# Kernel tuning notes

Hardware: AMD Instinct MI355X
Metric: run time of the kernel (lower is better)

## Reference

```python
import jax, jax.numpy as jnp
import numpy as np

N_NODES = 100000


def setup_inputs() -> dict:
    key = jax.random.key(0)
    ks = jax.random.split(key, 8)
    E = 1600000
    x = jax.random.normal(ks[0], (N_NODES, 128), dtype=jnp.float32)
    src = jax.random.randint(ks[1], (E,), 0, N_NODES, dtype=jnp.int32)
    dst = jax.random.randint(ks[2], (E,), 0, N_NODES, dtype=jnp.int32)
    s = 1.0 / np.sqrt(128.0)
    w_self = jax.random.normal(ks[3], (5, 128, 128), dtype=jnp.float32) * s
    w_neigh = jax.random.normal(ks[4], (5, 128, 128), dtype=jnp.float32) * s
    b = jnp.zeros((5, 128), dtype=jnp.float32)
    w_self_out = jax.random.normal(ks[5], (128, 47), dtype=jnp.float32) * s
    w_neigh_out = jax.random.normal(ks[6], (128, 47), dtype=jnp.float32) * s
    b_out = jnp.zeros((47,), dtype=jnp.float32)
    return {"x": x, "src": src, "dst": dst, "w_self": w_self, "w_neigh": w_neigh,
            "b": b, "w_self_out": w_self_out, "w_neigh_out": w_neigh_out, "b_out": b_out}


def _mean_agg(h, src, dst, inv_deg):
    # segment-sum of source features into destination nodes, then mean
    summed = jax.ops.segment_sum(h[src], dst, num_segments=N_NODES)  # [N, d]
    return summed * inv_deg[:, None]


def _sage_layer(h, src, dst, inv_deg, ws, wn, bias):
    neigh = _mean_agg(h, src, dst, inv_deg)
    return h @ ws + neigh @ wn + bias


def reference(x, src, dst, w_self, w_neigh, b, w_self_out, w_neigh_out, b_out):
    # in-degree, clamped to 1 for isolated nodes (DGL mean aggregator behavior)
    deg = jax.ops.segment_sum(jnp.ones_like(dst, dtype=x.dtype), dst, num_segments=N_NODES)
    inv_deg = 1.0 / jnp.maximum(deg, 1.0)

    # layer 0: no ReLU after (matches original forward)
    h = _sage_layer(x, src, dst, inv_deg, w_self[0], w_neigh[0], b[0])
    # layers 1..4: SAGEConv + ReLU
    for i in range(1, 5):
        h = _sage_layer(h, src, dst, inv_deg, w_self[i], w_neigh[i], b[i])
        h = jax.nn.relu(h)
    # final layer: 128 -> num_classes, no activation
    h = _sage_layer(h, src, dst, inv_deg, w_self_out, w_neigh_out, b_out)
    return h
```

## Files before the change

### kernel.cpp

```cpp
#include <hip/hip_runtime.h>

typedef float f4 __attribute__((ext_vector_type(4)));
typedef float f32x4 __attribute__((ext_vector_type(4)));
typedef short s16x8 __attribute__((ext_vector_type(8)));

#define N_NODES 100000
#define NBUCK 196
#define NB1 256

__device__ inline unsigned short f2bf(float f) {
    unsigned int u = __builtin_bit_cast(unsigned int, f);
    u += 0x7FFFu + ((u >> 16) & 1u);
    return (unsigned short)(u >> 16);
}
__device__ inline float bflo(unsigned int v) { return __builtin_bit_cast(float, v << 16); }
__device__ inline float bfhi(unsigned int v) { return __builtin_bit_cast(float, v & 0xFFFF0000u); }


__global__ __launch_bounds__(256) void k_hist(const int* __restrict__ dst,
                                              int* __restrict__ histG, int E) {
    __shared__ int h[NBUCK];
    int tid = threadIdx.x;
    for (int i = tid; i < NBUCK; i += 256) h[i] = 0;
    __syncthreads();
    int chunk = (E + NB1 - 1) / NB1;
    int s = blockIdx.x * chunk, eN = min(E, s + chunk);
    for (int i = s + tid; i < eN; i += 256) atomicAdd(&h[dst[i] >> 9], 1);
    __syncthreads();
    for (int i = tid; i < NBUCK; i += 256) histG[i * NB1 + blockIdx.x] = h[i];
}

__global__ __launch_bounds__(1024) void k_scanB(int* __restrict__ histG) {
    __shared__ int ps[1024];
    int t = threadIdx.x;
    int base = t * 49;
    int vals[49];
    int sum = 0;
#pragma unroll
    for (int i = 0; i < 49; ++i) { vals[i] = histG[base + i]; sum += vals[i]; }
    ps[t] = sum;
    __syncthreads();
    for (int off = 1; off < 1024; off <<= 1) {
        int v = (t >= off) ? ps[t - off] : 0;
        __syncthreads();
        ps[t] += v;
        __syncthreads();
    }
    int run = ps[t] - sum;
#pragma unroll
    for (int i = 0; i < 49; ++i) { int v = vals[i]; histG[base + i] = run; run += v; }
}

__global__ __launch_bounds__(256) void k_place(const int* __restrict__ src,
                                               const int* __restrict__ dst,
                                               const int* __restrict__ histG,
                                               unsigned int* __restrict__ ebuf, int E) {
    __shared__ int cur[NBUCK];
    int tid = threadIdx.x;
    for (int i = tid; i < NBUCK; i += 256) cur[i] = histG[i * NB1 + blockIdx.x];
    __syncthreads();
    int chunk = (E + NB1 - 1) / NB1;
    int s = blockIdx.x * chunk, eN = min(E, s + chunk);
    for (int i = s + tid; i < eN; i += 256) {
        int d = dst[i];
        int b = d >> 9;
        int pos = atomicAdd(&cur[b], 1);
        ebuf[pos] = (unsigned int)src[i] | ((unsigned int)(d & 511) << 17);
    }
}

__global__ __launch_bounds__(256) void k_csr(const unsigned int* __restrict__ ebuf,
                                             const int* __restrict__ histG,
                                             int* __restrict__ rp, int* __restrict__ col,
                                             float* __restrict__ invd, int N, int E) {
    __shared__ int ldeg[512];
    __shared__ int lbase[512];
    int b = blockIdx.x, tid = threadIdx.x;
    int base = histG[b * NB1];
    int endB = (b == NBUCK - 1) ? E : histG[(b + 1) * NB1];
    int cnt = endB - base;
    int n0 = b << 9;

    ldeg[tid] = 0;
    ldeg[tid + 256] = 0;
    __syncthreads();
    for (int i = tid; i < cnt; i += 256) atomicAdd(&ldeg[ebuf[base + i] >> 17], 1);
    __syncthreads();

    int a0 = ldeg[tid], a1 = ldeg[tid + 256];
    lbase[tid] = a0;
    lbase[tid + 256] = a1;
    __syncthreads();
    for (int off = 1; off < 512; off <<= 1) {
        int v0 = (tid >= off) ? lbase[tid - off] : 0;
        int v1 = (tid + 256 >= off) ? lbase[tid + 256 - off] : 0;
        __syncthreads();
        lbase[tid] += v0;
        lbase[tid + 256] += v1;
        __syncthreads();
    }
    int e0 = lbase[tid] - a0, e1 = lbase[tid + 256] - a1;
    __syncthreads();
    lbase[tid] = e0;
    lbase[tid + 256] = e1;
    ldeg[tid] = 0;
    ldeg[tid + 256] = 0;
    __syncthreads();

    for (int i = tid; i < cnt; i += 256) {
        unsigned int p = ebuf[base + i];
        int dl = p >> 17;
        int pos = base + lbase[dl] + atomicAdd(&ldeg[dl], 1);
        col[pos] = (int)(p & 0x1FFFFu);
    }

    int g0 = n0 + tid, g1 = n0 + tid + 256;
    if (g0 < N) { rp[g0] = base + e0; invd[g0] = 1.0f / fmaxf((float)a0, 1.0f); }
    if (g1 < N) { rp[g1] = base + e1; invd[g1] = 1.0f / fmaxf((float)a1, 1.0f); }
    if (b == NBUCK - 1 && tid == 0) rp[N] = E;
}


__global__ void k_cvt(const float* __restrict__ x, unsigned short* __restrict__ xb, int n8) {
    int t = blockIdx.x * 256 + threadIdx.x;
    if (t >= n8) return;
    f4 a = *(const f4*)&x[(size_t)t * 8];
    f4 b = *(const f4*)&x[(size_t)t * 8 + 4];
    s16x8 p;
    p[0] = (short)f2bf(a[0]); p[1] = (short)f2bf(a[1]);
    p[2] = (short)f2bf(a[2]); p[3] = (short)f2bf(a[3]);
    p[4] = (short)f2bf(b[0]); p[5] = (short)f2bf(b[1]);
    p[6] = (short)f2bf(b[2]); p[7] = (short)f2bf(b[3]);
    *(s16x8*)&xb[(size_t)t * 8] = p;
}

__global__ void k_prepw(const float* __restrict__ ws, const float* __restrict__ wn,
                        unsigned short* __restrict__ wp) {
    int t = blockIdx.x * 256 + threadIdx.x;
    if (t >= 5 * 4096) return;
    int l = t & 63, nfg = (t >> 6) & 7, ks = (t >> 9) & 7, lyr = t >> 12;
    int n = nfg * 16 + (l & 15);
    s16x8 p;
#pragma unroll
    for (int j = 0; j < 8; ++j) {
        int k = ks * 32 + (l >> 4) * 8 + j;
        float v = (k < 128) ? ws[((size_t)lyr * 128 + k) * 128 + n]
                            : wn[((size_t)lyr * 128 + (k - 128)) * 128 + n];
        p[j] = (short)f2bf(v);
    }
    *(s16x8*)&wp[(size_t)t * 8] = p;
}

__global__ void k_prepwo(const float* __restrict__ wso, const float* __restrict__ wno,
                         unsigned short* __restrict__ wpo) {
    int t = blockIdx.x * 256 + threadIdx.x;
    if (t >= 1536) return;
    int l = t & 63, q = t >> 6;
    int nf = q % 3, ks = q / 3;
    int n = nf * 16 + (l & 15);
    s16x8 p;
#pragma unroll
    for (int j = 0; j < 8; ++j) {
        int k = ks * 32 + (l >> 4) * 8 + j;
        float v = 0.f;
        if (n < 47) v = (k < 128) ? wso[(size_t)k * 47 + n] : wno[(size_t)(k - 128) * 47 + n];
        p[j] = (short)f2bf(v);
    }
    *(s16x8*)&wpo[(size_t)t * 8] = p;
}


__global__ __launch_bounds__(256) void k_agg(const unsigned short* __restrict__ h,
                                             const int* __restrict__ rp,
                                             const int* __restrict__ col,
                                             const float* __restrict__ invd,
                                             unsigned short* __restrict__ out, int n) {
    int gw = (blockIdx.x * 256 + threadIdx.x) >> 6;
    int lane = threadIdx.x & 63;
    if (gw >= n) return;
    const unsigned int* hp = (const unsigned int*)h;
    int beg = rp[gw], end = rp[gw + 1];
    float ax = 0.f, ay = 0.f;
    int e = beg;
    for (; e + 8 <= end; e += 8) {
        unsigned int u[8];
#pragma unroll
        for (int i = 0; i < 8; ++i) u[i] = hp[(size_t)col[e + i] * 64 + lane];
#pragma unroll
        for (int i = 0; i < 8; ++i) { ax += bflo(u[i]); ay += bfhi(u[i]); }
    }
    if (e < end) {
        int rem = end - e;
        unsigned int u[8];
#pragma unroll
        for (int i = 0; i < 8; ++i) {
            int idx = (i < rem) ? (e + i) : e;
            u[i] = hp[(size_t)col[idx] * 64 + lane];
        }
#pragma unroll
        for (int i = 0; i < 8; ++i) {
            if (i < rem) { ax += bflo(u[i]); ay += bfhi(u[i]); }
        }
    }
    float iv = invd[gw];
    unsigned int r = (unsigned int)f2bf(ax * iv) | ((unsigned int)f2bf(ay * iv) << 16);
    ((unsigned int*)out)[(size_t)gw * 64 + lane] = r;
}


__global__ __launch_bounds__(256) void gemm128(const unsigned short* __restrict__ h,
                                               const unsigned short* __restrict__ nb,
                                               const unsigned short* __restrict__ wl,
                                               const float* __restrict__ bias,
                                               unsigned short* __restrict__ out,
                                               int M, int relu) {
    __shared__ s16x8 afr[4096];
    const int tid = threadIdx.x;
    const int l = tid & 63, w = tid >> 6;
    const int r0 = blockIdx.x * 128;
    const int cg = (w * 4 + (l >> 4)) * 8;

    s16x8 th[8], tn[8];
#pragma unroll
    for (int i = 0; i < 8; ++i) {
        int r = r0 + i * 16 + (l & 15);
        if (r >= M) r = M - 1;
        th[i] = *(const s16x8*)(h + (size_t)r * 128 + cg);
        tn[i] = *(const s16x8*)(nb + (size_t)r * 128 + cg);
    }
#pragma unroll
    for (int i = 0; i < 8; ++i) {
        afr[(w * 8 + i) * 64 + l] = th[i];
        afr[((w + 4) * 8 + i) * 64 + l] = tn[i];
    }
    __syncthreads();

    const int mh = w >> 1, nh = w & 1;
    const s16x8* wf = (const s16x8*)wl;

    f32x4 acc[4][4];
#pragma unroll
    for (int i = 0; i < 4; ++i)
#pragma unroll
        for (int j = 0; j < 4; ++j) acc[i][j] = (f32x4)0.f;

#pragma unroll
    for (int ks = 0; ks < 8; ++ks) {
        s16x8 bw[4], ha[4];
#pragma unroll
        for (int nf = 0; nf < 4; ++nf) bw[nf] = wf[(ks * 8 + nh * 4 + nf) * 64 + l];
#pragma unroll
        for (int mf = 0; mf < 4; ++mf) ha[mf] = afr[(ks * 8 + mh * 4 + mf) * 64 + l];
#pragma unroll
        for (int mf = 0; mf < 4; ++mf)
#pragma unroll
            for (int nf = 0; nf < 4; ++nf)
                acc[mf][nf] = __builtin_amdgcn_mfma_f32_16x16x32_bf16(bw[nf], ha[mf],
                                                                      acc[mf][nf], 0, 0, 0);
    }

    f4 bv[4];
#pragma unroll
    for (int nf = 0; nf < 4; ++nf)
        bv[nf] = *(const f4*)&bias[nh * 64 + nf * 16 + ((l >> 4) << 2)];

#pragma unroll
    for (int mf = 0; mf < 4; ++mf) {
        int row = r0 + mh * 64 + mf * 16 + (l & 15);
        if (row >= M) continue;
#pragma unroll
        for (int nf = 0; nf < 4; ++nf) {
            int ncol = nh * 64 + nf * 16 + ((l >> 4) << 2);
            f32x4 a = acc[mf][nf];
            float v0 = a[0] + bv[nf][0], v1 = a[1] + bv[nf][1];
            float v2 = a[2] + bv[nf][2], v3 = a[3] + bv[nf][3];
            if (relu) {
                v0 = fmaxf(v0, 0.f); v1 = fmaxf(v1, 0.f);
                v2 = fmaxf(v2, 0.f); v3 = fmaxf(v3, 0.f);
            }
            uint2 p;
            p.x = (unsigned int)f2bf(v0) | ((unsigned int)f2bf(v1) << 16);
            p.y = (unsigned int)f2bf(v2) | ((unsigned int)f2bf(v3) << 16);
            *(uint2*)(out + (size_t)row * 128 + ncol) = p;
        }
    }
}


__global__ __launch_bounds__(256) void gemm_out47(const unsigned short* __restrict__ h,
                                                  const unsigned short* __restrict__ nb,
                                                  const unsigned short* __restrict__ wpo,
                                                  const float* __restrict__ bo,
                                                  float* __restrict__ out, int M) {
    __shared__ s16x8 afr[4096];
    const int tid = threadIdx.x;
    const int l = tid & 63, w = tid >> 6;
    const int r0 = blockIdx.x * 128;
    const int cg = (w * 4 + (l >> 4)) * 8;

    s16x8 th[8], tn[8];
#pragma unroll
    for (int i = 0; i < 8; ++i) {
        int r = r0 + i * 16 + (l & 15);
        if (r >= M) r = M - 1;
        th[i] = *(const s16x8*)(h + (size_t)r * 128 + cg);
        tn[i] = *(const s16x8*)(nb + (size_t)r * 128 + cg);
    }
#pragma unroll
    for (int i = 0; i < 8; ++i) {
        afr[(w * 8 + i) * 64 + l] = th[i];
        afr[((w + 4) * 8 + i) * 64 + l] = tn[i];
    }
    __syncthreads();

    const s16x8* wf = (const s16x8*)wpo;
    f32x4 acc[2][3];
#pragma unroll
    for (int i = 0; i < 2; ++i)
#pragma unroll
        for (int j = 0; j < 3; ++j) acc[i][j] = (f32x4)0.f;

#pragma unroll
    for (int ks = 0; ks < 8; ++ks) {
        s16x8 bw[3], ha[2];
#pragma unroll
        for (int nf = 0; nf < 3; ++nf) bw[nf] = wf[(ks * 3 + nf) * 64 + l];
#pragma unroll
        for (int mf = 0; mf < 2; ++mf) ha[mf] = afr[(ks * 8 + w * 2 + mf) * 64 + l];
#pragma unroll
        for (int mf = 0; mf < 2; ++mf)
#pragma unroll
            for (int nf = 0; nf < 3; ++nf)
                acc[mf][nf] = __builtin_amdgcn_mfma_f32_16x16x32_bf16(bw[nf], ha[mf],
                                                                      acc[mf][nf], 0, 0, 0);
    }

#pragma unroll
    for (int mf = 0; mf < 2; ++mf) {
        int row = r0 + w * 32 + mf * 16 + (l & 15);
        if (row >= M) continue;
#pragma unroll
        for (int nf = 0; nf < 3; ++nf) {
            int ncol = nf * 16 + ((l >> 4) << 2);
            f32x4 a = acc[mf][nf];
#pragma unroll
            for (int jj = 0; jj < 4; ++jj) {
                int n = ncol + jj;
                if (n < 47) out[(size_t)row * 47 + n] = a[jj] + bo[n];
            }
        }
    }
}


static inline char* alignp(char* p) {
    return (char*)(((size_t)p + 255) & ~(size_t)255);
}

extern "C" void kernel_launch(void* const* d_in, const int* in_sizes, int n_in,
                              void* d_out, int out_size, void* d_ws, size_t ws_size,
                              hipStream_t stream) {
    const float* x = (const float*)d_in[0];
    const int* src = (const int*)d_in[1];
    const int* dst = (const int*)d_in[2];
    const float* w_self = (const float*)d_in[3];
    const float* w_neigh = (const float*)d_in[4];
    const float* b = (const float*)d_in[5];
    const float* wso = (const float*)d_in[6];
    const float* wno = (const float*)d_in[7];
    const float* bo = (const float*)d_in[8];
    float* out = (float*)d_out;

    const int N = N_NODES;
    const int E = in_sizes[1];

    char* w = (char*)d_ws;
    unsigned short* xb = (unsigned short*)w;  w = alignp(w + (size_t)N * 128 * 2);
    unsigned short* hA = (unsigned short*)w;  w = alignp(w + (size_t)N * 128 * 2);
    unsigned short* hB = (unsigned short*)w;  w = alignp(w + (size_t)N * 128 * 2);
    unsigned short* wp = (unsigned short*)w;  w = alignp(w + (size_t)5 * 32768 * 2);
    unsigned short* wpo = (unsigned short*)w; w = alignp(w + (size_t)1536 * 8 * 2);
    int* rp = (int*)w;       w = alignp(w + (size_t)(N + 4) * 4);
    int* col = (int*)w;      w = alignp(w + (size_t)E * 4);
    int* histG = (int*)w;    w = alignp(w + (size_t)NBUCK * NB1 * 4);
    float* invd = (float*)w; w = alignp(w + (size_t)N * 4);

    unsigned int* ebuf = (unsigned int*)hB;

    k_hist<<<NB1, 256, 0, stream>>>(dst, histG, E);
    k_scanB<<<1, 1024, 0, stream>>>(histG);
    k_place<<<NB1, 256, 0, stream>>>(src, dst, histG, ebuf, E);
    k_csr<<<NBUCK, 256, 0, stream>>>(ebuf, histG, rp, col, invd, N, E);

    k_cvt<<<(N * 128 / 8 + 255) / 256, 256, 0, stream>>>(x, xb, N * 128 / 8);
    k_prepw<<<(5 * 4096 + 255) / 256, 256, 0, stream>>>(w_self, w_neigh, wp);
    k_prepwo<<<6, 256, 0, stream>>>(wso, wno, wpo);

    const int aggBlocks = (N * 64 + 255) / 256;
    const int gemmBlocks = (N + 127) / 128;

    k_agg<<<aggBlocks, 256, 0, stream>>>(xb, rp, col, invd, hA, N);
    gemm128<<<gemmBlocks, 256, 0, stream>>>(xb, hA, wp, b, hA, N, 0);

    unsigned short* cur = hA;
    unsigned short* oth = hB;
    for (int lyr = 1; lyr < 5; ++lyr) {
        k_agg<<<aggBlocks, 256, 0, stream>>>(cur, rp, col, invd, oth, N);
        gemm128<<<gemmBlocks, 256, 0, stream>>>(cur, oth, wp + (size_t)lyr * 32768,
                                                b + (size_t)lyr * 128, oth, N, 1);
        unsigned short* t = cur; cur = oth; oth = t;
    }

    k_agg<<<aggBlocks, 256, 0, stream>>>(cur, rp, col, invd, oth, N);
    gemm_out47<<<gemmBlocks, 256, 0, stream>>>(cur, oth, wpo, bo, out, N);
}
```

Baseline: 580.3 us.

## Fuse neighbor aggregation into the per-layer GEMM with LDS-staged neighbor tile

Replaces the separate aggregation and GEMM kernels with one fused kernel per layer. Each block gathers the mean of its 64 rows' neighbors into a swizzled LDS tile, then runs MFMA with self features read directly from global memory. Column indices are pre-shifted to byte offsets and padded so the gather can use 16-byte vector index loads. This removes the round trip of the aggregated tensor through global memory and one launch per layer. The cost is that the gather phase (latency bound) and the MFMA phase no longer overlap across kernels, and the gather loop now runs one row per wave sequentially.

```diff
diff --git a/kernel.cpp b/kernel.cpp
--- a/kernel.cpp
+++ b/kernel.cpp
@@ -2,7 +2,9 @@
 
 typedef float f4 __attribute__((ext_vector_type(4)));
 typedef float f32x4 __attribute__((ext_vector_type(4)));
+typedef float f2 __attribute__((ext_vector_type(2)));
 typedef short s16x8 __attribute__((ext_vector_type(8)));
+typedef int i4 __attribute__((ext_vector_type(4)));
 
 #define N_NODES 100000
 #define NBUCK 196
@@ -111,13 +113,14 @@
         unsigned int p = ebuf[base + i];
         int dl = p >> 17;
         int pos = base + lbase[dl] + atomicAdd(&ldeg[dl], 1);
-        col[pos] = (int)(p & 0x1FFFFu);
+        col[pos] = (int)(p & 0x1FFFFu) << 8;
     }
 
     int g0 = n0 + tid, g1 = n0 + tid + 256;
     if (g0 < N) { rp[g0] = base + e0; invd[g0] = 1.0f / fmaxf((float)a0, 1.0f); }
     if (g1 < N) { rp[g1] = base + e1; invd[g1] = 1.0f / fmaxf((float)a1, 1.0f); }
     if (b == NBUCK - 1 && tid == 0) rp[N] = E;
+    if (b == NBUCK - 1 && tid < 16) col[E + tid] = 0;
 }
 
 
@@ -170,89 +173,105 @@
 }
 
 
-__global__ __launch_bounds__(256) void k_agg(const unsigned short* __restrict__ h,
-                                             const int* __restrict__ rp,
-                                             const int* __restrict__ col,
-                                             const float* __restrict__ invd,
-                                             unsigned short* __restrict__ out, int n) {
-    int gw = (blockIdx.x * 256 + threadIdx.x) >> 6;
-    int lane = threadIdx.x & 63;
-    if (gw >= n) return;
-    const unsigned int* hp = (const unsigned int*)h;
-    int beg = rp[gw], end = rp[gw + 1];
-    float ax = 0.f, ay = 0.f;
+__device__ inline f2 gather_row(const char* hb, const int* __restrict__ col,
+                                int beg, int end, int lb) {
+    f2 a = {0.f, 0.f};
     int e = beg;
     for (; e + 8 <= end; e += 8) {
+        i4 c0, c1;
+        __builtin_memcpy(&c0, &col[e], 16);
+        __builtin_memcpy(&c1, &col[e + 4], 16);
         unsigned int u[8];
 #pragma unroll
-        for (int i = 0; i < 8; ++i) u[i] = hp[(size_t)col[e + i] * 64 + lane];
-#pragma unroll
-        for (int i = 0; i < 8; ++i) { ax += bflo(u[i]); ay += bfhi(u[i]); }
+        for (int j = 0; j < 4; ++j)
+            u[j] = *(const unsigned int*)(hb + (unsigned int)(c0[j] + lb));
+#pragma unroll
+        for (int j = 0; j < 4; ++j)
+            u[4 + j] = *(const unsigned int*)(hb + (unsigned int)(c1[j] + lb));
+#pragma unroll
+        for (int j = 0; j < 8; ++j) { f2 v = {bflo(u[j]), bfhi(u[j])}; a += v; }
+    }
+    for (; e + 4 <= end; e += 4) {
+        i4 c0;
+        __builtin_memcpy(&c0, &col[e], 16);
+        unsigned int u[4];
+#pragma unroll
+        for (int j = 0; j < 4; ++j)
+            u[j] = *(const unsigned int*)(hb + (unsigned int)(c0[j] + lb));
+#pragma unroll
+        for (int j = 0; j < 4; ++j) { f2 v = {bflo(u[j]), bfhi(u[j])}; a += v; }
     }
     if (e < end) {
         int rem = end - e;
-        unsigned int u[8];
-#pragma unroll
-        for (int i = 0; i < 8; ++i) {
-            int idx = (i < rem) ? (e + i) : e;
-            u[i] = hp[(size_t)col[idx] * 64 + lane];
+        i4 c0;
+        __builtin_memcpy(&c0, &col[e], 16);
+        unsigned int u[4];
+#pragma unroll
+        for (int j = 0; j < 4; ++j)
+            u[j] = *(const unsigned int*)(hb + (unsigned int)(c0[j] + lb));
+#pragma unroll
+        for (int j = 0; j < 4; ++j) {
+            if (j < rem) { f2 v = {bflo(u[j]), bfhi(u[j])}; a += v; }
         }
-#pragma unroll
-        for (int i = 0; i < 8; ++i) {
-            if (i < rem) { ax += bflo(u[i]); ay += bfhi(u[i]); }
+    }
+    return a;
+}
+
+
+__global__ __launch_bounds__(256, 4) void fused_layer(
+        const unsigned short* __restrict__ h,
+        const unsigned short* __restrict__ wl,
+        const float* __restrict__ bias,
+        const int* __restrict__ rp, const int* __restrict__ col,
+        const float* __restrict__ invd,
+        unsigned short* __restrict__ out, int M, int relu) {
+    __shared__ s16x8 nlds_v[1024];
+    char* nlds = (char*)nlds_v;
+    const int tid = threadIdx.x;
+    const int l = tid & 63, wv = tid >> 6;
+    const int r0 = blockIdx.x * 64;
+    const char* hb = (const char*)h;
+    const int lb = l * 4;
+
+    for (int i = 0; i < 16; ++i) {
+        int lr = wv * 16 + i;
+        int R = r0 + lr;
+        if (R > M - 1) R = M - 1;
+        f2 a = gather_row(hb, col, rp[R], rp[R + 1], lb);
+        float iv = invd[R];
+        unsigned int r = (unsigned int)f2bf(a[0] * iv) | ((unsigned int)f2bf(a[1] * iv) << 16);
+        *(unsigned int*)(nlds + lr * 256 + ((l * 4) ^ ((lr & 7) << 4))) = r;
+    }
+    __syncthreads();
+
+    const int mh = wv >> 1, nh = wv & 1;
+    const s16x8* wf = (const s16x8*)wl;
+
+    f32x4 acc[2][4];
+#pragma unroll
+    for (int i = 0; i < 2; ++i)
+#pragma unroll
+        for (int j = 0; j < 4; ++j) acc[i][j] = (f32x4)0.f;
+
+#pragma unroll
+    for (int ks = 0; ks < 8; ++ks) {
+        s16x8 bw[4], ha[2];
+#pragma unroll
+        for (int nf = 0; nf < 4; ++nf) bw[nf] = wf[(ks * 8 + nh * 4 + nf) * 64 + l];
+#pragma unroll
+        for (int mf = 0; mf < 2; ++mf) {
+            int lr = mh * 32 + mf * 16 + (l & 15);
+            if (ks < 4) {
+                int R = r0 + lr;
+                if (R > M - 1) R = M - 1;
+                ha[mf] = *(const s16x8*)(h + (size_t)R * 128 + ks * 32 + ((l >> 4) << 3));
+            } else {
+                int boff = ((ks - 4) << 6) + ((l >> 4) << 4);
+                ha[mf] = *(const s16x8*)(nlds + lr * 256 + (boff ^ ((lr & 7) << 4)));
+            }
         }
-    }
-    float iv = invd[gw];
-    unsigned int r = (unsigned int)f2bf(ax * iv) | ((unsigned int)f2bf(ay * iv) << 16);
-    ((unsigned int*)out)[(size_t)gw * 64 + lane] = r;
-}
-
-
-__global__ __launch_bounds__(256) void gemm128(const unsigned short* __restrict__ h,
-                                               const unsigned short* __restrict__ nb,
-                                               const unsigned short* __restrict__ wl,
-                                               const float* __restrict__ bias,
-                                               unsigned short* __restrict__ out,
-                                               int M, int relu) {
-    __shared__ s16x8 afr[4096];
-    const int tid = threadIdx.x;
-    const int l = tid & 63, w = tid >> 6;
-    const int r0 = blockIdx.x * 128;
-    const int cg = (w * 4 + (l >> 4)) * 8;
-
-    s16x8 th[8], tn[8];
-#pragma unroll
-    for (int i = 0; i < 8; ++i) {
-        int r = r0 + i * 16 + (l & 15);
-        if (r >= M) r = M - 1;
-        th[i] = *(const s16x8*)(h + (size_t)r * 128 + cg);
-        tn[i] = *(const s16x8*)(nb + (size_t)r * 128 + cg);
-    }
-#pragma unroll
-    for (int i = 0; i < 8; ++i) {
-        afr[(w * 8 + i) * 64 + l] = th[i];
-        afr[((w + 4) * 8 + i) * 64 + l] = tn[i];
-    }
-    __syncthreads();
-
-    const int mh = w >> 1, nh = w & 1;
-    const s16x8* wf = (const s16x8*)wl;
-
-    f32x4 acc[4][4];
-#pragma unroll
-    for (int i = 0; i < 4; ++i)
-#pragma unroll
-        for (int j = 0; j < 4; ++j) acc[i][j] = (f32x4)0.f;
-
-#pragma unroll
-    for (int ks = 0; ks < 8; ++ks) {
-        s16x8 bw[4], ha[4];
-#pragma unroll
-        for (int nf = 0; nf < 4; ++nf) bw[nf] = wf[(ks * 8 + nh * 4 + nf) * 64 + l];
-#pragma unroll
-        for (int mf = 0; mf < 4; ++mf) ha[mf] = afr[(ks * 8 + mh * 4 + mf) * 64 + l];
-#pragma unroll
-        for (int mf = 0; mf < 4; ++mf)
+#pragma unroll
+        for (int mf = 0; mf < 2; ++mf)
 #pragma unroll
             for (int nf = 0; nf < 4; ++nf)
                 acc[mf][nf] = __builtin_amdgcn_mfma_f32_16x16x32_bf16(bw[nf], ha[mf],
@@ -265,8 +284,8 @@
         bv[nf] = *(const f4*)&bias[nh * 64 + nf * 16 + ((l >> 4) << 2)];
 
 #pragma unroll
-    for (int mf = 0; mf < 4; ++mf) {
-        int row = r0 + mh * 64 + mf * 16 + (l & 15);
+    for (int mf = 0; mf < 2; ++mf) {
+        int row = r0 + mh * 32 + mf * 16 + (l & 15);
         if (row >= M) continue;
 #pragma unroll
         for (int nf = 0; nf < 4; ++nf) {
@@ -287,62 +306,62 @@
 }
 
 
-__global__ __launch_bounds__(256) void gemm_out47(const unsigned short* __restrict__ h,
-                                                  const unsigned short* __restrict__ nb,
-                                                  const unsigned short* __restrict__ wpo,
-                                                  const float* __restrict__ bo,
-                                                  float* __restrict__ out, int M) {
-    __shared__ s16x8 afr[4096];
+__global__ __launch_bounds__(256, 4) void fused_out(
+        const unsigned short* __restrict__ h,
+        const unsigned short* __restrict__ wpo,
+        const float* __restrict__ bo,
+        const int* __restrict__ rp, const int* __restrict__ col,
+        const float* __restrict__ invd,
+        float* __restrict__ out, int M) {
+    __shared__ s16x8 nlds_v[1024];
+    char* nlds = (char*)nlds_v;
     const int tid = threadIdx.x;
-    const int l = tid & 63, w = tid >> 6;
-    const int r0 = blockIdx.x * 128;
-    const int cg = (w * 4 + (l >> 4)) * 8;
-
-    s16x8 th[8], tn[8];
-#pragma unroll
-    for (int i = 0; i < 8; ++i) {
-        int r = r0 + i * 16 + (l & 15);
-        if (r >= M) r = M - 1;
-        th[i] = *(const s16x8*)(h + (size_t)r * 128 + cg);
-        tn[i] = *(const s16x8*)(nb + (size_t)r * 128 + cg);
-    }
-#pragma unroll
-    for (int i = 0; i < 8; ++i) {
-        afr[(w * 8 + i) * 64 + l] = th[i];
-        afr[((w + 4) * 8 + i) * 64 + l] = tn[i];
+    const int l = tid & 63, wv = tid >> 6;
+    const int r0 = blockIdx.x * 64;
+    const char* hb = (const char*)h;
+    const int lb = l * 4;
+
+    for (int i = 0; i < 16; ++i) {
+        int lr = wv * 16 + i;
+        int R = r0 + lr;
+        if (R > M - 1) R = M - 1;
+        f2 a = gather_row(hb, col, rp[R], rp[R + 1], lb);
+        float iv = invd[R];
+        unsigned int r = (unsigned int)f2bf(a[0] * iv) | ((unsigned int)f2bf(a[1] * iv) << 16);
+        *(unsigned int*)(nlds + lr * 256 + ((l * 4) ^ ((lr & 7) << 4))) = r;
     }
     __syncthreads();
 
     const s16x8* wf = (const s16x8*)wpo;
-    f32x4 acc[2][3];
-#pragma unroll
-    for (int i = 0; i < 2; ++i)
-#pragma unroll
-        for (int j = 0; j < 3; ++j) acc[i][j] = (f32x4)0.f;
-
+    f32x4 acc[3];
+#pragma unroll
+    for (int j = 0; j < 3; ++j) acc[j] = (f32x4)0.f;
+
+    const int lr0 = wv * 16 + (l & 15);
 #pragma unroll
     for (int ks = 0; ks < 8; ++ks) {
-        s16x8 bw[3], ha[2];
+        s16x8 bw[3], ha;
 #pragma unroll
         for (int nf = 0; nf < 3; ++nf) bw[nf] = wf[(ks * 3 + nf) * 64 + l];
-#pragma unroll
-        for (int mf = 0; mf < 2; ++mf) ha[mf] = afr[(ks * 8 + w * 2 + mf) * 64 + l];
-#pragma unroll
-        for (int mf = 0; mf < 2; ++mf)
-#pragma unroll
-            for (int nf = 0; nf < 3; ++nf)
-                acc[mf][nf] = __builtin_amdgcn_mfma_f32_16x16x32_bf16(bw[nf], ha[mf],
-                                                                      acc[mf][nf], 0, 0, 0);
-    }
-
-#pragma unroll
-    for (int mf = 0; mf < 2; ++mf) {
-        int row = r0 + w * 32 + mf * 16 + (l & 15);
-        if (row >= M) continue;
+        if (ks < 4) {
+            int R = r0 + lr0;
+            if (R > M - 1) R = M - 1;
+            ha = *(const s16x8*)(h + (size_t)R * 128 + ks * 32 + ((l >> 4) << 3));
+        } else {
+            int boff = ((ks - 4) << 6) + ((l >> 4) << 4);
+            ha = *(const s16x8*)(nlds + lr0 * 256 + (boff ^ ((lr0 & 7) << 4)));
+        }
+#pragma unroll
+        for (int nf = 0; nf < 3; ++nf)
+            acc[nf] = __builtin_amdgcn_mfma_f32_16x16x32_bf16(bw[nf], ha, acc[nf], 0, 0, 0);
+    }
+
+    int row = r0 + lr0;
+    if (row < M) {
 #pragma unroll
         for (int nf = 0; nf < 3; ++nf) {
             int ncol = nf * 16 + ((l >> 4) << 2);
-            f32x4 a = acc[mf][nf];
+            f32x4 a = acc[nf];
 #pragma unroll
             for (int jj = 0; jj < 4; ++jj) {
                 int n = ncol + jj;
@@ -381,7 +400,7 @@
     unsigned short* wp = (unsigned short*)w;  w = alignp(w + (size_t)5 * 32768 * 2);
     unsigned short* wpo = (unsigned short*)w; w = alignp(w + (size_t)1536 * 8 * 2);
     int* rp = (int*)w;       w = alignp(w + (size_t)(N + 4) * 4);
-    int* col = (int*)w;      w = alignp(w + (size_t)E * 4);
+    int* col = (int*)w;      w = alignp(w + (size_t)(E + 16) * 4);
     int* histG = (int*)w;    w = alignp(w + (size_t)NBUCK * NB1 * 4);
     float* invd = (float*)w; w = alignp(w + (size_t)N * 4);
 
@@ -396,21 +415,18 @@
     k_prepw<<<(5 * 4096 + 255) / 256, 256, 0, stream>>>(w_self, w_neigh, wp);
     k_prepwo<<<6, 256, 0, stream>>>(wso, wno, wpo);
 
-    const int aggBlocks = (N * 64 + 255) / 256;
-    const int gemmBlocks = (N + 127) / 128;
-
-    k_agg<<<aggBlocks, 256, 0, stream>>>(xb, rp, col, invd, hA, N);
-    gemm128<<<gemmBlocks, 256, 0, stream>>>(xb, hA, wp, b, hA, N, 0);
+    const int fusedBlocks = (N + 63) / 64;
+
+    fused_layer<<<fusedBlocks, 256, 0, stream>>>(xb, wp, b, rp, col, invd, hA, N, 0);
 
     unsigned short* cur = hA;
     unsigned short* oth = hB;
     for (int lyr = 1; lyr < 5; ++lyr) {
-        k_agg<<<aggBlocks, 256, 0, stream>>>(cur, rp, col, invd, oth, N);
-        gemm128<<<gemmBlocks, 256, 0, stream>>>(cur, oth, wp + (size_t)lyr * 32768,
-                                                b + (size_t)lyr * 128, oth, N, 1);
+        fused_layer<<<fusedBlocks, 256, 0, stream>>>(cur, wp + (size_t)lyr * 32768,
+                                                     b + (size_t)lyr * 128,
+                                                     rp, col, invd, oth, N, 1);
         unsigned short* t = cur; cur = oth; oth = t;
     }
 
-    k_agg<<<aggBlocks, 256, 0, stream>>>(cur, rp, col, invd, oth, N);
-    gemm_out47<<<gemmBlocks, 256, 0, stream>>>(cur, oth, wpo, bo, out, N);
-}
+    fused_out<<<fusedBlocks, 256, 0, stream>>>(cur, wpo, bo, rp, col, invd, out, N);
+}
```

Result: slower. 696.1 us (+19.9%).
